# Kernel optimization log

Measured on AMD Instinct MI355X. Metric: run time of the kernel, lower is better.

## Reference

```python
import jax, jax.numpy as jnp
import numpy as np
from jax.scipy.linalg import solve_triangular

T, DZ, DX = 4096, 64, 64


def setup_inputs() -> dict:
    key = jax.random.key(0)
    ks = jax.random.split(key, 8)
    observations = jax.random.normal(ks[0], (T, DX), jnp.float32)
    # stable transition matrix (spectral radius < 1)
    A = 0.9 * jnp.eye(DZ, dtype=jnp.float32) + (0.05 / np.sqrt(DZ)) * jax.random.normal(ks[1], (DZ, DZ), jnp.float32)
    b = 0.01 * jax.random.normal(ks[2], (DZ,), jnp.float32)
    qf = jax.random.normal(ks[3], (DZ, DZ), jnp.float32) / np.sqrt(DZ)
    Q = qf @ qf.T + 0.1 * jnp.eye(DZ, dtype=jnp.float32)  # SPD process noise
    H = jax.random.normal(ks[4], (DX, DZ), jnp.float32) / np.sqrt(DZ)
    c = 0.01 * jax.random.normal(ks[5], (DX,), jnp.float32)
    rf = jax.random.normal(ks[6], (DX, DX), jnp.float32) / np.sqrt(DX)
    R = rf @ rf.T + 0.1 * jnp.eye(DX, dtype=jnp.float32)  # SPD observation noise
    prior_mean = jnp.zeros((DZ,), jnp.float32)
    prior_cov = jnp.eye(DZ, dtype=jnp.float32)
    return dict(observations=observations, A=A, b=b, Q=Q, H=H, c=c, R=R,
                prior_mean=prior_mean, prior_cov=prior_cov)


def _update(m, P, y, H, c, R):
    # Kalman update + Gaussian log-likelihood term (stable Cholesky form of
    # the torch.inverse / MultivariateNormal math).
    yhat = H @ m + c                      # predicted obs mean
    S = H @ P @ H.T + R                   # innovation covariance [dx,dx]
    K = jnp.linalg.solve(S, H @ P).T      # gain = P H^T S^{-1} (S, P symmetric)
    r = y - yhat
    fm = m + K @ r
    fP = P - K @ H @ P
    L = jnp.linalg.cholesky(S)
    z = solve_triangular(L, r, lower=True)
    dx = y.shape[0]
    ll = (-0.5 * dx * jnp.log(2.0 * jnp.pi)
          - jnp.sum(jnp.log(jnp.diag(L)))
          - 0.5 * jnp.sum(z * z))
    return fm, fP, ll


def reference(observations, A, b, Q, H, c, R, prior_mean, prior_cov):
    # ---- filter ----
    fm0, fP0, ll0 = _update(prior_mean, prior_cov, observations[0], H, c, R)

    def fstep(carry, y):
        m, P = carry
        pm = A @ m + b                    # predict
        pP = A @ P @ A.T + Q
        fm, fP, ll = _update(pm, pP, y, H, c, R)
        return (fm, fP), (pm, pP, fm, fP, ll)

    _, (pms, pPs, fms, fPs, lls) = jax.lax.scan(fstep, (fm0, fP0), observations[1:])
    pm = jnp.concatenate([prior_mean[None], pms])   # [T, dz]
    pP = jnp.concatenate([prior_cov[None], pPs])    # [T, dz, dz]
    fm = jnp.concatenate([fm0[None], fms])
    fP = jnp.concatenate([fP0[None], fPs])
    loglikelihood = ll0 + jnp.sum(lls)

    # ---- RTS smoother (backward recursion) ----
    def bstep(carry, xs):
        sm, sP = carry
        fmt, fPt, pmn, pPn = xs
        C = jnp.linalg.solve(pPn, A @ fPt).T          # fP A^T pP^{-1}
        sm_t = fmt + C @ (sm - pmn)
        sP_t = fPt + C @ (sP - pPn) @ C.T
        return (sm_t, sP_t), (sm_t, sP_t)

    _, (sms, sPs) = jax.lax.scan(bstep, (fm[-1], fP[-1]),
                                 (fm[:-1], fP[:-1], pm[1:], pP[1:]), reverse=True)
    smoothed_means = jnp.concatenate([sms, fm[-1][None]])
    smoothed_covs = jnp.concatenate([sPs, fP[-1][None]])
    return smoothed_means, smoothed_covs, loglikelihood
```

## Files before the change

kernel.cpp:

```cpp
#include <hip/hip_runtime.h>
#include <math.h>

#define NN 64
#define LDW 68
#define LCH 32
#define N1CAP 144
#define N0MAX 144
#define EPS_HARD 1e-5f
#define EPS_GATE 5e-2f
#define STALL_WIN 5
#define STALL_IMP 0.75f

struct KP {
  const float *Y, *A, *b, *Q, *H, *c, *R, *pm0, *P0;
  float *out_mean, *out_cov, *out_ll;
  int *meta; float *metaF;
  float *fm;
  float *AT, *HT, *HA, *Hb;
  float *Fss, *Kss, *Sinvss, *Css, *CsTss, *pPss, *sPss, *Fpow, *Cpow32, *Cpow31, *uss;
  float *Pw2, *Pw4, *Pw8, *Pw16, *Pw64, *Pw128;
  float *FpwHi, *CpwHi;
  float *Dmss, *dvnss;
  float *u_chunk, *startstate, *ub_chunk, *endstate;
  float *scanF0, *scanF1, *scanB0, *scanB1;
  float *ld_pref, *u_pref;
  double *llbuf;
  float *E0g;
  float *EA, *EC, *EJ, *EL;
  float *astat, *dstat;
  float *scM0, *scM1, *scG0, *scG1;
  float *fP, *pP, *Kp, *Sinvp, *Fp, *Cp, *CsTp, *Dmp, *dvnp;
  int N0cap, T, NC;
};

union F4 { float4 v; float f[4]; };


__device__ __forceinline__ void g2l(float* W, const float* G) {
  for (int e = threadIdx.x*4; e < 4096; e += 1024) {
    float4 v = *(const float4*)(G + e);
    *(float4*)(W + (e>>6)*LDW + (e&63)) = v;
  }
  __syncthreads();
}
__device__ __forceinline__ void l2g(float* G, const float* W) {
  for (int e = threadIdx.x*4; e < 4096; e += 1024)
    *(float4*)(G + e) = *(const float4*)(W + (e>>6)*LDW + (e&63));
  __syncthreads();
}
__device__ __forceinline__ void l2g2(float* G1, const float* Wa,
                                     float* G2, const float* Wb) {
  for (int e = threadIdx.x*4; e < 4096; e += 1024) {
    int base = (e>>6)*LDW + (e&63);
    *(float4*)(G1 + e) = *(const float4*)(Wa + base);
    *(float4*)(G2 + e) = *(const float4*)(Wb + base);
  }
// ... 699 lines not shown
  const int t = blockIdx.x;
  if (t >= N0) return;
  mm<0,0,0,LDW>(W1, P.H, NN, P.pP + (size_t)t*4096, NN, nullptr, 0);
  mm<0,0,1,LDW>(CH, W1, LDW, P.HT, NN, P.R, NN);
  chol68<true>(CH, part, invd);
  if (tid == 0) { float s=0.f; for (int j=0;j<64;++j) s += part[j]; P.ld_pref[t] = s; }
  set_id(W0);
  tri_s2x2(CH, invd, W1, W0);
  l2g_T(P.Kp + (size_t)t*4096, W1);
  if (tid < 64) {
    float s = P.b[tid];
    for (int k = 0; k < 64; ++k) s -= W1[k*LDW + tid]*P.Hb[k];
    P.u_pref[t*64 + tid] = s;
  }
  __syncthreads();
  l2g(P.Sinvp + (size_t)t*4096, W0);
  mm<1,0,2,LDW>(W0, W1, LDW, P.HA, NN, P.A, NN);
  l2g(P.Fp + (size_t)t*4096, W0);
  mm<0,0,0,LDW>(W1, P.A, NN, P.fP + (size_t)t*4096, NN, nullptr, 0);
  g2l(CH, P.pP + (size_t)(t+1)*4096);
  chol68<false>(CH, part, invd);
  tri_solve2(CH, invd, W1, W1);
  l2g(P.CsTp + (size_t)t*4096, W1);
  l2g_T(P.Cp + (size_t)t*4096, W1);
  mm<1,0,0,LDW>(W0, W1, LDW, P.A, NN, nullptr, 0);
  store_id_sub(P.Dmp + (size_t)t*4096, W0);
  if (tid < 64) {
    float s = 0.f;
    for (int k = 0; k < 64; ++k) s += W1[k*LDW + tid]*P.b[k];
    P.dvnp[t*64 + tid] = -s;
  }
}

__global__ __launch_bounds__(256) void k1y(KP P) {
  __shared__ __align__(16) float W0[LDW*NN], W1[LDW*NN], W2[LDW*NN], W3[LDW*NN], W4[LDW*NN], CH[LDW*NN];
  const int N0 = P.meta[0];
  const float* fPssG = P.fP + (size_t)(N0-1)*4096;
  if (blockIdx.x == 0) {
    mm2<0,0,0,LDW, 0,0,0,LDW>(W1, P.Css,NN, P.Css,NN, nullptr,0,
                              W4, P.Fss,NN, P.Fss,NN, nullptr,0);
    l2g(P.Pw2, W1);
    mm2<0,0,0,LDW, 0,0,0,LDW>(W2, W1,LDW, W1,LDW, nullptr,0,
                              W3, W4,LDW, W4,LDW, nullptr,0);
    l2g(P.Pw4, W2);
    mm2<0,0,0,LDW, 0,0,0,LDW>(W0, W2,LDW, W2,LDW, nullptr,0,
                              W4, W3,LDW, W3,LDW, nullptr,0);
    l2g(P.Pw8, W0);
    mm2<0,0,0,LDW, 0,0,0,LDW>(W1, W0,LDW, W0,LDW, nullptr,0,
                              W3, W4,LDW, W4,LDW, nullptr,0);
    l2g(P.Pw16, W1);
    mm2<0,0,0,LDW, 0,0,0,LDW>(W2, W1,LDW, W1,LDW, nullptr,0,
                              W4, W3,LDW, W3,LDW, nullptr,0);
    l2g2(P.Cpow32, W2, P.Fpow, W4);
    mm2<0,0,0,LDW, 0,0,0,LDW>(W0, W2,LDW, W2,LDW, nullptr,0,
                              W3, W4,LDW, W4,LDW, nullptr,0);
    l2g2(P.Pw64, W0, P.FpwHi, W3);
    mm2<0,0,0,LDW, 0,0,0,LDW>(W1, W0,LDW, W0,LDW, nullptr,0,
                              W4, W3,LDW, W3,LDW, nullptr,0);
    l2g2(P.Pw128, W1, P.FpwHi + 4096, W4);
    mm2<0,0,0,LDW, 0,0,0,LDW>(W2, W1,LDW, W1,LDW, nullptr,0,
                              W3, W4,LDW, W4,LDW, nullptr,0);
    l2g2(P.CpwHi, W2, P.FpwHi + 2*4096, W3);
    mm2<0,0,0,LDW, 0,0,0,LDW>(W0, W2,LDW, W2,LDW, nullptr,0,
                              W4, W3,LDW, W3,LDW, nullptr,0);
    l2g2(P.CpwHi + 4096, W0, P.FpwHi + 3*4096, W4);
    mm2<0,0,0,LDW, 0,0,0,LDW>(W1, W0,LDW, W0,LDW, nullptr,0,
                              W3, W4,LDW, W4,LDW, nullptr,0);
    l2g2(P.CpwHi + 2*4096, W1, P.FpwHi + 4*4096, W3);
    mm2<0,0,0,LDW, 0,0,0,LDW>(W2, W1,LDW, W1,LDW, nullptr,0,
                              W4, W3,LDW, W3,LDW, nullptr,0);
    l2g2(P.CpwHi + 3*4096, W2, P.FpwHi + 5*4096, W4);
    mm<0,0,0,LDW>(W0, P.Pw16, NN, P.Pw8, NN, nullptr, 0);
    mm<0,0,0,LDW>(W1, W0, LDW, P.Pw4, NN, nullptr, 0);
    mm<0,0,0,LDW>(W2, W1, LDW, P.Pw2, NN, nullptr, 0);
    mm<0,0,0,LDW>(W0, W2, LDW, P.Css, NN, nullptr, 0);
    l2g(P.Cpow31, W0);
  } else {
    g2l(W1, P.Css);
    g2l(W2, P.CsTss);
    g2l(W0, P.pPss);
    mm<0,0,0,LDW>(CH, W1, LDW, W0, LDW, nullptr, 0);
    mm<0,0,2,LDW>(W0, CH, LDW, W2, LDW, fPssG, NN);
    float *m1 = W1, *m2 = W2, *t1 = W3, *t2 = W4;
    for (int it = 0; it < 7; ++it) {
      mm2<0,0,0,LDW, 0,0,0,LDW>(CH, m1,LDW, W0,LDW, nullptr,0,
                                t1, m1,LDW, m1,LDW, nullptr,0);
      mm2<0,0,1,LDW, 0,0,0,LDW>(W0, CH,LDW, m2,LDW, W0,LDW,
                                t2, m2,LDW, m2,LDW, nullptr,0);
      float* tmp = m1; m1 = t1; t1 = tmp;
      tmp = m2; m2 = t2; t2 = tmp;
    }
    l2g(P.sPss, W0);
    rsub_store(P.E0g, fPssG, W0);
  }
}

__global__ __launch_bounds__(256) void kTail(KP P) {
  __shared__ __align__(16) float W0[LDW*NN], W1[LDW*NN], W2[LDW*NN];
  const int t = blockIdx.x;
  const int N0 = P.meta[0];
  if (t < N0) return;
  float* dst = P.out_cov + (size_t)t*4096;
  if (t < P.T - N1CAP) {
    for (int e = threadIdx.x*4; e < 4096; e += 1024)
      *(float4*)(dst+e) = *(const float4*)(P.sPss + e);
    return;
  }
  const int k = P.T - 1 - t;
  if (k == 0) {
    const float* src = P.fP + (size_t)(N0-1)*4096;
    for (int e = threadIdx.x*4; e < 4096; e += 1024)
      *(float4*)(dst+e) = *(const float4*)(src+e);
    return;
  }
  const float* pw[8] = {P.Css, P.Pw2, P.Pw4, P.Pw8, P.Pw16, P.Cpow32, P.Pw64, P.Pw128};
  int b = __ffs(k) - 1;
  g2l(W1, pw[b]);
  float* cur = W1; float* oth = W0;
  for (int j = b+1; j < 8; ++j) {
    if ((k >> j) & 1) {
      mm<0,0,0,LDW>(oth, pw[j], NN, cur, LDW, nullptr, 0);
      float* tmp = cur; cur = oth; oth = tmp;
    }
  }
  mm<0,0,0,LDW>(W2, cur, LDW, P.E0g, NN, nullptr, 0);
  mm<0,1,1,LDW>(oth, W2, LDW, cur, LDW, P.sPss, NN);
  l2g(dst, oth);
}

__global__ __launch_bounds__(256) void k1cI(KP P) {
  __shared__ __align__(16) float W1[LDW*NN];
  const int t = blockIdx.x;
  if (t >= P.meta[0]) return;
  const float* Cg = P.Cp + (size_t)t*4096;
  for (int e = threadIdx.x*4; e < 4096; e += 1024)
    *(float4*)(P.scM0 + (size_t)t*4096 + e) = *(const float4*)(Cg + e);
  mm<0,0,0,LDW>(W1, Cg, NN, P.pP + (size_t)(t+1)*4096, NN, nullptr, 0);
  mm<0,0,2,NN>(P.scG0 + (size_t)t*4096, W1, LDW,
               P.CsTp + (size_t)t*4096, NN, P.fP + (size_t)t*4096, NN);
}

__global__ __launch_bounds__(256) void k1cL(KP P, int step, int sidx) {
  __shared__ __align__(16) float W1[LDW*NN];
  const int t = blockIdx.x;
  const int N0 = P.meta[0];
  if (t >= N0) return;
  const float* Msrc = sidx ? P.scM1 : P.scM0;
  const float* Gsrc = sidx ? P.scG1 : P.scG0;
  float* Mdst = sidx ? P.scM0 : P.scM1;
  float* Gdst = sidx ? P.scG0 : P.scG1;
  const int s = t + step;
  if (s >= N0) {
    for (int e = threadIdx.x*4; e < 4096; e += 1024) {
      *(float4*)(Mdst + (size_t)t*4096 + e) = *(const float4*)(Msrc + (size_t)t*4096 + e);
      *(float4*)(Gdst + (size_t)t*4096 + e) = *(const float4*)(Gsrc + (size_t)t*4096 + e);
    }
    return;
  }
  const float* Mt = Msrc + (size_t)t*4096;
  mm2<0,0,0,LDW, 0,0,0,NN>(W1, Mt,NN, Gsrc + (size_t)s*4096,NN, nullptr,0,
                           Mdst + (size_t)t*4096, Mt,NN, Msrc + (size_t)s*4096,NN, nullptr,0);
  mm<0,1,1,NN>(Gdst + (size_t)t*4096, W1, LDW, Mt, NN, Gsrc + (size_t)t*4096, NN);
}

__global__ __launch_bounds__(256) void k1cF(KP P) {
  __shared__ __align__(16) float W1[LDW*NN];
  const int t = blockIdx.x;
  if (t >= P.meta[0]) return;
  const float* Mt = P.scM0 + (size_t)t*4096;
  mm<0,0,0,LDW>(W1, Mt, NN, P.sPss, NN, nullptr, 0);
  mm<0,1,1,NN>(P.out_cov + (size_t)t*4096, W1, LDW, Mt, NN,
               P.scG0 + (size_t)t*4096, NN);
}

__global__ __launch_bounds__(256) void k2a(KP P) {
  __shared__ float xv[64], ty[64], red[256];
  const int c = blockIdx.x;
  const int N0 = P.meta[0];
  const int PB = (N0 + LCH - 1)/LCH;
  if (c < PB) return;
  const int tid = threadIdx.x;
  if (tid < 64) xv[tid] = 0.f;
  __syncthreads();
  for (int s = 0; s < LCH; ++s) {
    int t = c*LCH + s;
    if (tid < 64) ty[tid] = P.Y[(size_t)t*64+tid] - P.c[tid];
    __syncthreads();
    matvec2(xv, P.Fss, xv, P.Kss, ty, P.uss, red);
  }
  if (tid < 64) P.scanF0[(size_t)(c+1)*64 + tid] = xv[tid];
}

__global__ __launch_bounds__(256) void k2b(KP P) {
  __shared__ float xv[64], ty[64], hp[64], red[256];
  const int tid = threadIdx.x;
  const int N0 = P.meta[0];
  const int PB = (N0 + LCH - 1)/LCH;
  const int PE = PB*LCH;
  if (tid < 64) xv[tid] = P.pm0[tid];
  __syncthreads();
  matvec256(hp, P.H, xv, nullptr, red);
  if (tid < 64) ty[tid] = P.Y[tid] - hp[tid] - P.c[tid];
  __syncthreads();
  matvec256(xv, P.Kp, ty, xv, red);
  if (tid < 64) P.fm[tid] = xv[tid];
  __syncthreads();
  for (int t = 1; t < PE; ++t) {
    const float* Kt = (t < N0) ? P.Kp + (size_t)t*4096 : P.Kss;
    const float* Ft = (t < N0) ? P.Fp + (size_t)t*4096 : P.Fss;
    const float* ut = (t < N0) ? P.u_pref + t*64 : P.uss;
    if (tid < 64) ty[tid] = P.Y[(size_t)t*64+tid] - P.c[tid];
    __syncthreads();
    matvec2(xv, Ft, xv, Kt, ty, ut, red);
    if (tid < 64) P.fm[(size_t)t*64+tid] = xv[tid];
    __syncthreads();
  }
  if (tid < 64) P.scanF0[(size_t)PB*64 + tid] = xv[tid];
}

__global__ __launch_bounds__(64) void k2s(KP P, int j) {
  const int c = blockIdx.x;
  const int N0 = P.meta[0];
  const int PB = (N0 + LCH - 1)/LCH;
  if (c < PB) return;
  const int sidx = j & 1;
  const float* src = sidx ? P.scanF1 : P.scanF0;
  float* dst = sidx ? P.scanF0 : P.scanF1;
  const int off = 1 << j;
  const int r = threadIdx.x;
  float base = src[(size_t)c*64 + r];
  if (c - off >= PB) {
    __shared__ float xv[64];
    xv[r] = src[(size_t)(c-off)*64 + r];
    __syncthreads();
    const float* M = (j == 0) ? P.Fpow : P.FpwHi + (size_t)(j-1)*4096;
    const float* Mr = M + r*64;
    float s = base;
    for (int k = 0; k < 64; k += 4)
      s += Mr[k]*xv[k] + Mr[k+1]*xv[k+1] + Mr[k+2]*xv[k+2] + Mr[k+3]*xv[k+3];
    dst[(size_t)c*64 + r] = s;
  } else {
    dst[(size_t)c*64 + r] = base;
  }
}

__global__ __launch_bounds__(256) void k2c(KP P) {
  __shared__ float xv[64], ty[64], red[256];
  const int c = blockIdx.x;
  const int N0 = P.meta[0];
  const int PB = (N0 + LCH - 1)/LCH;
  if (c < PB) return;
  const int tid = threadIdx.x;
  if (tid < 64) xv[tid] = P.scanF1[(size_t)c*64 + tid];
  __syncthreads();
  for (int s = 0; s < LCH; ++s) {
    int t = c*LCH + s;
    if (tid < 64) ty[tid] = P.Y[(size_t)t*64+tid] - P.c[tid];
    __syncthreads();
    matvec2(xv, P.Fss, xv, P.Kss, ty, P.uss, red);
    if (tid < 64) P.fm[(size_t)t*64+tid] = xv[tid];
    __syncthreads();
  }
}

__global__ __launch_bounds__(64) void k5(KP P) {
  __shared__ float pmv[64], rv[64];
  const int t = blockIdx.x;
  const int N0 = P.meta[0];
  const int r = threadIdx.x;
  float pm;
  if (t == 0) {
    pm = P.pm0[r];
  } else {
    pmv[r] = P.fm[(size_t)(t-1)*64 + r];
    __syncthreads();
    float s = P.b[r];
    const float* Ar = P.A + r*64;
    for (int k = 0; k < 64; k += 4)
      s += Ar[k]*pmv[k] + Ar[k+1]*pmv[k+1] + Ar[k+2]*pmv[k+2] + Ar[k+3]*pmv[k+3];
    pm = s;
    __syncthreads();
  }
  pmv[r] = pm; __syncthreads();
  float rr = P.Y[(size_t)t*64 + r] - P.c[r];
  const float* Hr = P.H + r*64;
  for (int k = 0; k < 64; ++k) rr -= Hr[k]*pmv[k];
  rv[r] = rr; __syncthreads();
  const float* Sv = ((t < N0) ? P.Sinvp + (size_t)t*4096 : P.Sinvss) + r*64;
  float wv = 0.f;
  for (int k = 0; k < 64; ++k) wv += Sv[k]*rv[k];
  float qq = rr*wv;
  #pragma unroll
  for (int off = 32; off > 0; off >>= 1) qq += __shfl_xor(qq, off, 64);
  if (r == 0) {
    float ldt = (t < N0) ? P.ld_pref[t] : P.metaF[0];
    P.llbuf[t] = -58.8120661250990555 - (double)ldt - 0.5*(double)qq;
  }
}

__global__ __launch_bounds__(256) void k3a(KP P) {
  __shared__ float sv[64], fmv[64], red[256];
  const int c = blockIdx.x;
  const int N0 = P.meta[0];
  const int PB = (N0 + LCH - 1)/LCH;
  if (c < PB) return;
  const int tid = threadIdx.x;
  if (tid < 64) sv[tid] = 0.f;
  __syncthreads();
  int hi = (c == P.NC-1) ? P.T-2 : c*LCH + LCH - 1;
  for (int t = hi; t >= c*LCH; --t) {
    if (tid < 64) fmv[tid] = P.fm[(size_t)t*64+tid];
    __syncthreads();
    matvec2(sv, P.Css, sv, P.Dmss, fmv, P.dvnss, red);
  }
  if (c == P.NC-1) {
    if (tid < 64) fmv[tid] = P.fm[(size_t)(P.T-1)*64 + tid];
    __syncthreads();
    matvec256(sv, P.Cpow31, fmv, sv, red);
  }
  if (tid < 64) P.scanB0[(size_t)c*64 + tid] = sv[tid];
}

__global__ __launch_bounds__(64) void k3s(KP P, int j) {
  const int c = blockIdx.x;
  const int N0 = P.meta[0];
  const int PB = (N0 + LCH - 1)/LCH;
  if (c < PB) return;
  const int sidx = j & 1;
  const float* src = sidx ? P.scanB1 : P.scanB0;
  float* dst = sidx ? P.scanB0 : P.scanB1;
  const int off = 1 << j;
  const int r = threadIdx.x;
  float base = src[(size_t)c*64 + r];
  if (c + off <= P.NC - 1) {
    __shared__ float xv[64];
    xv[r] = src[(size_t)(c+off)*64 + r];
    __syncthreads();
    const float* M;
    if (j == 0) M = P.Cpow32;
    else if (j == 1) M = P.Pw64;
    else if (j == 2) M = P.Pw128;
    else M = P.CpwHi + (size_t)(j-3)*4096;
    const float* Mr = M + r*64;
    float s = base;
    for (int k = 0; k < 64; k += 4)
      s += Mr[k]*xv[k] + Mr[k+1]*xv[k+1] + Mr[k+2]*xv[k+2] + Mr[k+3]*xv[k+3];
    dst[(size_t)c*64 + r] = s;
  } else {
    dst[(size_t)c*64 + r] = base;
  }
}

__global__ __launch_bounds__(256) void k3b(KP P) {
  __shared__ float sv[64], fmv[64], red[256];
  const int tid = threadIdx.x;
  const int N0 = P.meta[0];
  const int PB = (N0 + LCH - 1)/LCH;
  const int PE = PB*LCH;
  if (tid < 64) {
    P.out_mean[(size_t)(P.T-1)*64+tid] = P.fm[(size_t)(P.T-1)*64+tid];
    sv[tid] = P.scanB1[(size_t)PB*64 + tid];
  }
  __syncthreads();
  for (int t = PE-1; t >= 0; --t) {
    const float* Ct  = (t < N0) ? P.Cp  + (size_t)t*4096 : P.Css;
    const float* Dmt = (t < N0) ? P.Dmp + (size_t)t*4096 : P.Dmss;
    const float* dvt = (t < N0) ? P.dvnp + t*64 : P.dvnss;
    if (tid < 64) fmv[tid] = P.fm[(size_t)t*64+tid];
    __syncthreads();
    matvec2(sv, Ct, sv, Dmt, fmv, dvt, red);
    if (tid < 64) P.out_mean[(size_t)t*64+tid] = sv[tid];
    __syncthreads();
  }
}

__global__ __launch_bounds__(256) void k3c(KP P) {
  __shared__ float sv[64], fmv[64], red[256];
  const int c = blockIdx.x;
  const int N0 = P.meta[0];
  const int PB = (N0 + LCH - 1)/LCH;
  if (c < PB) return;
  const int tid = threadIdx.x;
  if (tid < 64) {
    sv[tid] = (c == P.NC-1) ? P.fm[(size_t)(P.T-1)*64+tid]
                            : P.scanB1[(size_t)(c+1)*64 + tid];
  }
  __syncthreads();
  int hi = (c == P.NC-1) ? P.T-2 : c*LCH + LCH - 1;
  for (int t = hi; t >= c*LCH; --t) {
    if (tid < 64) fmv[tid] = P.fm[(size_t)t*64+tid];
    __syncthreads();
    matvec2(sv, P.Css, sv, P.Dmss, fmv, P.dvnss, red);
    if (tid < 64) P.out_mean[(size_t)t*64+tid] = sv[tid];
    __syncthreads();
  }
}

__global__ __launch_bounds__(256) void k6(KP P) {
  __shared__ double rd[256];
  double s = 0.0;
  for (int t = threadIdx.x; t < P.T; t += 256) s += P.llbuf[t];
  rd[threadIdx.x] = s; __syncthreads();
  #pragma unroll
  for (int off = 128; off > 0; off >>= 1) {
    if ((int)threadIdx.x < off) rd[threadIdx.x] += rd[threadIdx.x + off];
    __syncthreads();
  }
  if (threadIdx.x == 0) P.out_ll[0] = (float)rd[0];
}


extern "C" void kernel_launch(void* const* d_in, const int* in_sizes, int n_in,
                              void* d_out, int out_size, void* d_ws, size_t ws_size,
                              hipStream_t stream) {
  (void)n_in; (void)out_size;
  KP P;
  P.Y   = (const float*)d_in[0];
  P.A   = (const float*)d_in[1];
  P.b   = (const float*)d_in[2];
  P.Q   = (const float*)d_in[3];
  P.H   = (const float*)d_in[4];
  P.c   = (const float*)d_in[5];
  P.R   = (const float*)d_in[6];
  P.pm0 = (const float*)d_in[7];
  P.P0  = (const float*)d_in[8];
  const int T = in_sizes[0] / 64;
  const int NC = T / LCH;
  P.T = T; P.NC = NC;

  float* out = (float*)d_out;
  P.out_mean = out;
  P.out_cov  = out + (size_t)T*64;
  P.out_ll   = out + (size_t)T*64 + (size_t)T*4096;

  float* w = (float*)d_ws;
  size_t off = 0;
  auto alloc = [&](size_t n) { float* p = w + off; off += n; return p; };
  P.meta   = (int*)alloc(8);
  P.metaF  = alloc(8);
  P.llbuf  = (double*)alloc((size_t)2*T);
  P.fm     = alloc((size_t)T*64);
  P.AT = alloc(4096); P.HT = alloc(4096); P.HA = alloc(4096); P.Hb = alloc(64);
  P.Fss = alloc(4096); P.Kss = alloc(4096); P.Sinvss = alloc(4096);
  P.Css = alloc(4096); P.CsTss = alloc(4096); P.pPss = alloc(4096); P.sPss = alloc(4096);
  P.Fpow = alloc(4096); P.Cpow32 = alloc(4096); P.Cpow31 = alloc(4096); P.uss = alloc(64);
  P.Pw2 = alloc(4096); P.Pw4 = alloc(4096); P.Pw8 = alloc(4096); P.Pw16 = alloc(4096);
  P.Pw64 = alloc(4096); P.Pw128 = alloc(4096);
  P.FpwHi = alloc((size_t)6*4096); P.CpwHi = alloc((size_t)4*4096);
  P.Dmss = alloc(4096); P.dvnss = alloc(64);
  P.u_chunk = alloc((size_t)NC*64); P.startstate = alloc((size_t)NC*64);
  P.ub_chunk = alloc((size_t)NC*64); P.endstate = alloc((size_t)NC*64);
  P.scanF0 = alloc((size_t)(NC+1)*64); P.scanF1 = alloc((size_t)(NC+1)*64);
  P.scanB0 = alloc((size_t)NC*64); P.scanB1 = alloc((size_t)NC*64);
  P.E0g = alloc(4096);
  P.EA = alloc((size_t)8*4096); P.EC = alloc((size_t)8*4096);
  P.EJ = alloc((size_t)8*4096); P.EL = alloc((size_t)8*4096);
  P.astat = alloc(256); P.dstat = alloc(256);
  size_t fixed = off;
  size_t per_t = 12*4096 + 128 + 1;
  size_t total_f = ws_size / 4;
  long long avail = (long long)total_f - (long long)fixed - 4096 - 64;
  int cap = (avail > 0) ? (int)(avail / (long long)per_t) : 8;
  if (cap > N0MAX) cap = N0MAX;
  if (cap < 8) cap = 8;
  P.N0cap = cap;
  P.ld_pref = alloc(cap);
  P.u_pref  = alloc((size_t)cap*64);
  P.dvnp    = alloc((size_t)cap*64);
  P.fP    = alloc((size_t)cap*4096);
  P.pP    = alloc((size_t)(cap+1)*4096);
  P.Kp    = alloc((size_t)cap*4096);
  P.Sinvp = alloc((size_t)cap*4096);
  P.Fp    = alloc((size_t)cap*4096);
  P.Cp    = alloc((size_t)cap*4096);
  P.CsTp  = alloc((size_t)cap*4096);
  P.Dmp   = alloc((size_t)cap*4096);
  P.scM0  = alloc((size_t)cap*4096);
  P.scM1  = alloc((size_t)cap*4096);
  P.scG0  = alloc((size_t)cap*4096);
  P.scG1  = alloc((size_t)cap*4096);

  k0<<<1, 256, 0, stream>>>(P);
  kA<<<1, 256, 0, stream>>>(P);
  kB<<<cap, 256, 0, stream>>>(P);
  kC<<<cap, 256, 0, stream>>>(P);
  kN<<<1, 256, 0, stream>>>(P);
  k1x<<<cap+1, 256, 0, stream>>>(P);
  k1y<<<2, 256, 0, stream>>>(P);
  k1cI<<<cap, 256, 0, stream>>>(P);
  {
    int sidx = 0;
    for (int d = 0; d < 8; ++d) { k1cL<<<cap, 256, 0, stream>>>(P, 1 << d, sidx); sidx ^= 1; }
  }
  k1cF<<<cap, 256, 0, stream>>>(P);
  kTail<<<T, 256, 0, stream>>>(P);
  k2a<<<NC, 256, 0, stream>>>(P);
  k2b<<<1, 256, 0, stream>>>(P);
  for (int j = 0; j < 7; ++j) k2s<<<NC, 64, 0, stream>>>(P, j);
  k2c<<<NC, 256, 0, stream>>>(P);
  k5<<<T, 64, 0, stream>>>(P);
  k3a<<<NC, 256, 0, stream>>>(P);
  for (int j = 0; j < 7; ++j) k3s<<<NC, 64, 0, stream>>>(P, j);
  k3b<<<1, 256, 0, stream>>>(P);
  k3c<<<NC, 256, 0, stream>>>(P);
  k6<<<1, 256, 0, stream>>>(P);
}
```

Measured before the change: 1.794 ms.

## Merge independent smoother and filter stages into combined multi-role kernels

Independent phases (power precomputation, steady-state covariance, chunked forward filter, covariance scan init, the prefix-scan levels, tail covariances, log-likelihood terms, backward smoother and final reduction) are packed into shared launches. Different block-index ranges take different roles, so independent work runs concurrently and roughly 30 launches shrink to about 18. Some previously parallel work now shares a launch with long serial single-block loops (the forward filter recursion now sits in the first combined kernel). Every block also reserves the largest shared-memory footprint, which may lower occupancy, and the larger grids add idle early-exit blocks.

Result: faster. 1.511 ms (median of 2 runs) (-15.8%).

```diff
diff --git a/kernel.cpp b/kernel.cpp
--- a/kernel.cpp
+++ b/kernel.cpp
@@ -21,7 +21,6 @@
   float *Pw2, *Pw4, *Pw8, *Pw16, *Pw64, *Pw128;
   float *FpwHi, *CpwHi;
   float *Dmss, *dvnss;
-  float *u_chunk, *startstate, *ub_chunk, *endstate;
   float *scanF0, *scanF1, *scanB0, *scanB1;
   float *ld_pref, *u_pref;
   double *llbuf;
@@ -787,293 +786,313 @@
   }
 }
 
-__global__ __launch_bounds__(256) void k1y(KP P) {
+__global__ __launch_bounds__(256) void mega0(KP P) {
   __shared__ __align__(16) float W0[LDW*NN], W1[LDW*NN], W2[LDW*NN], W3[LDW*NN], W4[LDW*NN], CH[LDW*NN];
-  const int N0 = P.meta[0];
-  const float* fPssG = P.fP + (size_t)(N0-1)*4096;
-  if (blockIdx.x == 0) {
-    mm2<0,0,0,LDW, 0,0,0,LDW>(W1, P.Css,NN, P.Css,NN, nullptr,0,
-                              W4, P.Fss,NN, P.Fss,NN, nullptr,0);
-    l2g(P.Pw2, W1);
-    mm2<0,0,0,LDW, 0,0,0,LDW>(W2, W1,LDW, W1,LDW, nullptr,0,
-                              W3, W4,LDW, W4,LDW, nullptr,0);
-    l2g(P.Pw4, W2);
-    mm2<0,0,0,LDW, 0,0,0,LDW>(W0, W2,LDW, W2,LDW, nullptr,0,
-                              W4, W3,LDW, W3,LDW, nullptr,0);
-    l2g(P.Pw8, W0);
-    mm2<0,0,0,LDW, 0,0,0,LDW>(W1, W0,LDW, W0,LDW, nullptr,0,
-                              W3, W4,LDW, W4,LDW, nullptr,0);
-    l2g(P.Pw16, W1);
-    mm2<0,0,0,LDW, 0,0,0,LDW>(W2, W1,LDW, W1,LDW, nullptr,0,
-                              W4, W3,LDW, W3,LDW, nullptr,0);
-    l2g2(P.Cpow32, W2, P.Fpow, W4);
-    mm2<0,0,0,LDW, 0,0,0,LDW>(W0, W2,LDW, W2,LDW, nullptr,0,
-                              W3, W4,LDW, W4,LDW, nullptr,0);
-    l2g2(P.Pw64, W0, P.FpwHi, W3);
-    mm2<0,0,0,LDW, 0,0,0,LDW>(W1, W0,LDW, W0,LDW, nullptr,0,
-                              W4, W3,LDW, W3,LDW, nullptr,0);
-    l2g2(P.Pw128, W1, P.FpwHi + 4096, W4);
-    mm2<0,0,0,LDW, 0,0,0,LDW>(W2, W1,LDW, W1,LDW, nullptr,0,
-                              W3, W4,LDW, W4,LDW, nullptr,0);
-    l2g2(P.CpwHi, W2, P.FpwHi + 2*4096, W3);
-    mm2<0,0,0,LDW, 0,0,0,LDW>(W0, W2,LDW, W2,LDW, nullptr,0,
-                              W4, W3,LDW, W3,LDW, nullptr,0);
-    l2g2(P.CpwHi + 4096, W0, P.FpwHi + 3*4096, W4);
-    mm2<0,0,0,LDW, 0,0,0,LDW>(W1, W0,LDW, W0,LDW, nullptr,0,
-                              W3, W4,LDW, W4,LDW, nullptr,0);
-    l2g2(P.CpwHi + 2*4096, W1, P.FpwHi + 4*4096, W3);
-    mm2<0,0,0,LDW, 0,0,0,LDW>(W2, W1,LDW, W1,LDW, nullptr,0,
-                              W4, W3,LDW, W3,LDW, nullptr,0);
-    l2g2(P.CpwHi + 3*4096, W2, P.FpwHi + 5*4096, W4);
-    mm<0,0,0,LDW>(W0, P.Pw16, NN, P.Pw8, NN, nullptr, 0);
-    mm<0,0,0,LDW>(W1, W0, LDW, P.Pw4, NN, nullptr, 0);
-    mm<0,0,0,LDW>(W2, W1, LDW, P.Pw2, NN, nullptr, 0);
-    mm<0,0,0,LDW>(W0, W2, LDW, P.Css, NN, nullptr, 0);
-    l2g(P.Cpow31, W0);
-  } else {
-    g2l(W1, P.Css);
-    g2l(W2, P.CsTss);
-    g2l(W0, P.pPss);
-    mm<0,0,0,LDW>(CH, W1, LDW, W0, LDW, nullptr, 0);
-    mm<0,0,2,LDW>(W0, CH, LDW, W2, LDW, fPssG, NN);
-    float *m1 = W1, *m2 = W2, *t1 = W3, *t2 = W4;
-    for (int it = 0; it < 7; ++it) {
-      mm2<0,0,0,LDW, 0,0,0,LDW>(CH, m1,LDW, W0,LDW, nullptr,0,
-                                t1, m1,LDW, m1,LDW, nullptr,0);
-      mm2<0,0,1,LDW, 0,0,0,LDW>(W0, CH,LDW, m2,LDW, W0,LDW,
-                                t2, m2,LDW, m2,LDW, nullptr,0);
-      float* tmp = m1; m1 = t1; t1 = tmp;
-      tmp = m2; m2 = t2; t2 = tmp;
-    }
-    l2g(P.sPss, W0);
-    rsub_store(P.E0g, fPssG, W0);
-  }
-}
-
-__global__ __launch_bounds__(256) void kTail(KP P) {
-  __shared__ __align__(16) float W0[LDW*NN], W1[LDW*NN], W2[LDW*NN];
-  const int t = blockIdx.x;
-  const int N0 = P.meta[0];
-  if (t < N0) return;
-  float* dst = P.out_cov + (size_t)t*4096;
-  if (t < P.T - N1CAP) {
-    for (int e = threadIdx.x*4; e < 4096; e += 1024)
-      *(float4*)(dst+e) = *(const float4*)(P.sPss + e);
-    return;
-  }
-  const int k = P.T - 1 - t;
-  if (k == 0) {
-    const float* src = P.fP + (size_t)(N0-1)*4096;
-    for (int e = threadIdx.x*4; e < 4096; e += 1024)
-      *(float4*)(dst+e) = *(const float4*)(src+e);
-    return;
-  }
-  const float* pw[8] = {P.Css, P.Pw2, P.Pw4, P.Pw8, P.Pw16, P.Cpow32, P.Pw64, P.Pw128};
-  int b = __ffs(k) - 1;
-  g2l(W1, pw[b]);
-  float* cur = W1; float* oth = W0;
-  for (int j = b+1; j < 8; ++j) {
-    if ((k >> j) & 1) {
-      mm<0,0,0,LDW>(oth, pw[j], NN, cur, LDW, nullptr, 0);
-      float* tmp = cur; cur = oth; oth = tmp;
-    }
-  }
-  mm<0,0,0,LDW>(W2, cur, LDW, P.E0g, NN, nullptr, 0);
-  mm<0,1,1,LDW>(oth, W2, LDW, cur, LDW, P.sPss, NN);
-  l2g(dst, oth);
-}
-
-__global__ __launch_bounds__(256) void k1cI(KP P) {
-  __shared__ __align__(16) float W1[LDW*NN];
-  const int t = blockIdx.x;
-  if (t >= P.meta[0]) return;
-  const float* Cg = P.Cp + (size_t)t*4096;
-  for (int e = threadIdx.x*4; e < 4096; e += 1024)
-    *(float4*)(P.scM0 + (size_t)t*4096 + e) = *(const float4*)(Cg + e);
-  mm<0,0,0,LDW>(W1, Cg, NN, P.pP + (size_t)(t+1)*4096, NN, nullptr, 0);
-  mm<0,0,2,NN>(P.scG0 + (size_t)t*4096, W1, LDW,
-               P.CsTp + (size_t)t*4096, NN, P.fP + (size_t)t*4096, NN);
-}
-
-__global__ __launch_bounds__(256) void k1cL(KP P, int step, int sidx) {
-  __shared__ __align__(16) float W1[LDW*NN];
-  const int t = blockIdx.x;
-  const int N0 = P.meta[0];
-  if (t >= N0) return;
-  const float* Msrc = sidx ? P.scM1 : P.scM0;
-  const float* Gsrc = sidx ? P.scG1 : P.scG0;
-  float* Mdst = sidx ? P.scM0 : P.scM1;
-  float* Gdst = sidx ? P.scG0 : P.scG1;
-  const int s = t + step;
-  if (s >= N0) {
-    for (int e = threadIdx.x*4; e < 4096; e += 1024) {
-      *(float4*)(Mdst + (size_t)t*4096 + e) = *(const float4*)(Msrc + (size_t)t*4096 + e);
-      *(float4*)(Gdst + (size_t)t*4096 + e) = *(const float4*)(Gsrc + (size_t)t*4096 + e);
-    }
-    return;
-  }
-  const float* Mt = Msrc + (size_t)t*4096;
-  mm2<0,0,0,LDW, 0,0,0,NN>(W1, Mt,NN, Gsrc + (size_t)s*4096,NN, nullptr,0,
-                           Mdst + (size_t)t*4096, Mt,NN, Msrc + (size_t)s*4096,NN, nullptr,0);
-  mm<0,1,1,NN>(Gdst + (size_t)t*4096, W1, LDW, Mt, NN, Gsrc + (size_t)t*4096, NN);
-}
-
-__global__ __launch_bounds__(256) void k1cF(KP P) {
-  __shared__ __align__(16) float W1[LDW*NN];
-  const int t = blockIdx.x;
-  if (t >= P.meta[0]) return;
-  const float* Mt = P.scM0 + (size_t)t*4096;
-  mm<0,0,0,LDW>(W1, Mt, NN, P.sPss, NN, nullptr, 0);
-  mm<0,1,1,NN>(P.out_cov + (size_t)t*4096, W1, LDW, Mt, NN,
-               P.scG0 + (size_t)t*4096, NN);
-}
-
-__global__ __launch_bounds__(256) void k2a(KP P) {
-  __shared__ float xv[64], ty[64], red[256];
-  const int c = blockIdx.x;
+  __shared__ float xv[64], ty[64], hp[64], red[256];
+  const int tid = threadIdx.x;
+  const int bid = blockIdx.x;
   const int N0 = P.meta[0];
   const int PB = (N0 + LCH - 1)/LCH;
-  if (c < PB) return;
+  if (bid == 0) {
+    const int PE = PB*LCH;
+    if (tid < 64) xv[tid] = P.pm0[tid];
+    __syncthreads();
+    matvec256(hp, P.H, xv, nullptr, red);
+    if (tid < 64) ty[tid] = P.Y[tid] - hp[tid] - P.c[tid];
+    __syncthreads();
+    matvec256(xv, P.Kp, ty, xv, red);
+    if (tid < 64) P.fm[tid] = xv[tid];
+    __syncthreads();
+    for (int t = 1; t < PE; ++t) {
+      const float* Kt = (t < N0) ? P.Kp + (size_t)t*4096 : P.Kss;
+      const float* Ft = (t < N0) ? P.Fp + (size_t)t*4096 : P.Fss;
+      const float* ut = (t < N0) ? P.u_pref + t*64 : P.uss;
+      if (tid < 64) ty[tid] = P.Y[(size_t)t*64+tid] - P.c[tid];
+      __syncthreads();
+      matvec2(xv, Ft, xv, Kt, ty, ut, red);
+      if (tid < 64) P.fm[(size_t)t*64+tid] = xv[tid];
+      __syncthreads();
+    }
+    if (tid < 64) P.scanF0[(size_t)PB*64 + tid] = xv[tid];
+  } else if (bid <= 2) {
+    const float* fPssG = P.fP + (size_t)(N0-1)*4096;
+    if (bid == 1) {
+      mm2<0,0,0,LDW, 0,0,0,LDW>(W1, P.Css,NN, P.Css,NN, nullptr,0,
+                                W4, P.Fss,NN, P.Fss,NN, nullptr,0);
+      l2g(P.Pw2, W1);
+      mm2<0,0,0,LDW, 0,0,0,LDW>(W2, W1,LDW, W1,LDW, nullptr,0,
+                                W3, W4,LDW, W4,LDW, nullptr,0);
+      l2g(P.Pw4, W2);
+      mm2<0,0,0,LDW, 0,0,0,LDW>(W0, W2,LDW, W2,LDW, nullptr,0,
+                                W4, W3,LDW, W3,LDW, nullptr,0);
+      l2g(P.Pw8, W0);
+      mm2<0,0,0,LDW, 0,0,0,LDW>(W1, W0,LDW, W0,LDW, nullptr,0,
+                                W3, W4,LDW, W4,LDW, nullptr,0);
+      l2g(P.Pw16, W1);
+      mm2<0,0,0,LDW, 0,0,0,LDW>(W2, W1,LDW, W1,LDW, nullptr,0,
+                                W4, W3,LDW, W3,LDW, nullptr,0);
+      l2g2(P.Cpow32, W2, P.Fpow, W4);
+      mm2<0,0,0,LDW, 0,0,0,LDW>(W0, W2,LDW, W2,LDW, nullptr,0,
+                                W3, W4,LDW, W4,LDW, nullptr,0);
+      l2g2(P.Pw64, W0, P.FpwHi, W3);
+      mm2<0,0,0,LDW, 0,0,0,LDW>(W1, W0,LDW, W0,LDW, nullptr,0,
+                                W4, W3,LDW, W3,LDW, nullptr,0);
+      l2g2(P.Pw128, W1, P.FpwHi + 4096, W4);
+      mm2<0,0,0,LDW, 0,0,0,LDW>(W2, W1,LDW, W1,LDW, nullptr,0,
+                                W3, W4,LDW, W4,LDW, nullptr,0);
+      l2g2(P.CpwHi, W2, P.FpwHi + 2*4096, W3);
+      mm2<0,0,0,LDW, 0,0,0,LDW>(W0, W2,LDW, W2,LDW, nullptr,0,
+                                W4, W3,LDW, W3,LDW, nullptr,0);
+      l2g2(P.CpwHi + 4096, W0, P.FpwHi + 3*4096, W4);
+      mm2<0,0,0,LDW, 0,0,0,LDW>(W1, W0,LDW, W0,LDW, nullptr,0,
+                                W3, W4,LDW, W4,LDW, nullptr,0);
+      l2g2(P.CpwHi + 2*4096, W1, P.FpwHi + 4*4096, W3);
+      mm2<0,0,0,LDW, 0,0,0,LDW>(W2, W1,LDW, W1,LDW, nullptr,0,
+                                W4, W3,LDW, W3,LDW, nullptr,0);
+      l2g2(P.CpwHi + 3*4096, W2, P.FpwHi + 5*4096, W4);
+      mm<0,0,0,LDW>(W0, P.Pw16, NN, P.Pw8, NN, nullptr, 0);
+      mm<0,0,0,LDW>(W1, W0, LDW, P.Pw4, NN, nullptr, 0);
+      mm<0,0,0,LDW>(W2, W1, LDW, P.Pw2, NN, nullptr, 0);
+      mm<0,0,0,LDW>(W0, W2, LDW, P.Css, NN, nullptr, 0);
+      l2g(P.Cpow31, W0);
+    } else {
+      g2l(W1, P.Css);
+      g2l(W2, P.CsTss);
+      g2l(W0, P.pPss);
+      mm<0,0,0,LDW>(CH, W1, LDW, W0, LDW, nullptr, 0);
+      mm<0,0,2,LDW>(W0, CH, LDW, W2, LDW, fPssG, NN);
+      float *m1 = W1, *m2 = W2, *t1 = W3, *t2 = W4;
+      for (int it = 0; it < 7; ++it) {
+        mm2<0,0,0,LDW, 0,0,0,LDW>(CH, m1,LDW, W0,LDW, nullptr,0,
+                                  t1, m1,LDW, m1,LDW, nullptr,0);
+        mm2<0,0,1,LDW, 0,0,0,LDW>(W0, CH,LDW, m2,LDW, W0,LDW,
+                                  t2, m2,LDW, m2,LDW, nullptr,0);
+        float* tmp = m1; m1 = t1; t1 = tmp;
+        tmp = m2; m2 = t2; t2 = tmp;
+      }
+      l2g(P.sPss, W0);
+      rsub_store(P.E0g, fPssG, W0);
+    }
+  } else if (bid < 3 + P.NC) {
+    const int c = bid - 3;
+    if (c < PB) return;
+    if (tid < 64) xv[tid] = 0.f;
+    __syncthreads();
+    for (int s = 0; s < LCH; ++s) {
+      int t = c*LCH + s;
+      if (tid < 64) ty[tid] = P.Y[(size_t)t*64+tid] - P.c[tid];
+      __syncthreads();
+      matvec2(xv, P.Fss, xv, P.Kss, ty, P.uss, red);
+    }
+    if (tid < 64) P.scanF0[(size_t)(c+1)*64 + tid] = xv[tid];
+  } else {
+    const int t = bid - 3 - P.NC;
+    if (t >= N0) return;
+    const float* Cg = P.Cp + (size_t)t*4096;
+    for (int e = tid*4; e < 4096; e += 1024)
+      *(float4*)(P.scM0 + (size_t)t*4096 + e) = *(const float4*)(Cg + e);
+    mm<0,0,0,LDW>(W1, Cg, NN, P.pP + (size_t)(t+1)*4096, NN, nullptr, 0);
+    mm<0,0,2,NN>(P.scG0 + (size_t)t*4096, W1, LDW,
+                 P.CsTp + (size_t)t*4096, NN, P.fP + (size_t)t*4096, NN);
+  }
+}
+
+__global__ __launch_bounds__(256) void megaL(KP P, int d) {
+  __shared__ __align__(16) float W1[LDW*NN];
+  __shared__ float xv[64];
   const int tid = threadIdx.x;
-  if (tid < 64) xv[tid] = 0.f;
-  __syncthreads();
-  for (int s = 0; s < LCH; ++s) {
-    int t = c*LCH + s;
-    if (tid < 64) ty[tid] = P.Y[(size_t)t*64+tid] - P.c[tid];
-    __syncthreads();
-    matvec2(xv, P.Fss, xv, P.Kss, ty, P.uss, red);
-  }
-  if (tid < 64) P.scanF0[(size_t)(c+1)*64 + tid] = xv[tid];
-}
-
-__global__ __launch_bounds__(256) void k2b(KP P) {
-  __shared__ float xv[64], ty[64], hp[64], red[256];
+  const int bid = blockIdx.x;
+  const int cap = P.N0cap;
+  const int N0 = P.meta[0];
+  if (bid < cap) {
+    const int t = bid;
+    if (t >= N0) return;
+    const int step = 1 << d, sidx = d & 1;
+    const float* Msrc = sidx ? P.scM1 : P.scM0;
+    const float* Gsrc = sidx ? P.scG1 : P.scG0;
+    float* Mdst = sidx ? P.scM0 : P.scM1;
+    float* Gdst = sidx ? P.scG0 : P.scG1;
+    const int s = t + step;
+    if (s >= N0) {
+      for (int e = tid*4; e < 4096; e += 1024) {
+        *(float4*)(Mdst + (size_t)t*4096 + e) = *(const float4*)(Msrc + (size_t)t*4096 + e);
+        *(float4*)(Gdst + (size_t)t*4096 + e) = *(const float4*)(Gsrc + (size_t)t*4096 + e);
+      }
+      return;
+    }
+    const float* Mt = Msrc + (size_t)t*4096;
+    mm2<0,0,0,LDW, 0,0,0,NN>(W1, Mt,NN, Gsrc + (size_t)s*4096,NN, nullptr,0,
+                             Mdst + (size_t)t*4096, Mt,NN, Msrc + (size_t)s*4096,NN, nullptr,0);
+    mm<0,1,1,NN>(Gdst + (size_t)t*4096, W1, LDW, Mt, NN, Gsrc + (size_t)t*4096, NN);
+  } else {
+    const int c = bid - cap;
+    const int PB = (N0 + LCH - 1)/LCH;
+    if (c < PB) return;
+    const int sidx = d & 1;
+    const float* src = sidx ? P.scanF1 : P.scanF0;
+    float* dst = sidx ? P.scanF0 : P.scanF1;
+    const int off = 1 << d;
+    const int r = tid;
+    if (c - off >= PB) {
+      if (r < 64) xv[r] = src[(size_t)(c-off)*64 + r];
+      __syncthreads();
+      if (r < 64) {
+        const float* M = (d == 0) ? P.Fpow : P.FpwHi + (size_t)(d-1)*4096;
+        const float* Mr = M + r*64;
+        float s = src[(size_t)c*64 + r];
+        for (int k = 0; k < 64; k += 4)
+          s += Mr[k]*xv[k] + Mr[k+1]*xv[k+1] + Mr[k+2]*xv[k+2] + Mr[k+3]*xv[k+3];
+        dst[(size_t)c*64 + r] = s;
+      }
+    } else {
+      if (r < 64) dst[(size_t)c*64 + r] = src[(size_t)c*64 + r];
+    }
+  }
+}
+
+__global__ __launch_bounds__(256) void megaL7(KP P) {
+  __shared__ __align__(16) float W1[LDW*NN];
+  __shared__ float xv[64], ty[64], red[256];
   const int tid = threadIdx.x;
+  const int bid = blockIdx.x;
   const int N0 = P.meta[0];
   const int PB = (N0 + LCH - 1)/LCH;
-  const int PE = PB*LCH;
-  if (tid < 64) xv[tid] = P.pm0[tid];
-  __syncthreads();
-  matvec256(hp, P.H, xv, nullptr, red);
-  if (tid < 64) ty[tid] = P.Y[tid] - hp[tid] - P.c[tid];
-  __syncthreads();
-  matvec256(xv, P.Kp, ty, xv, red);
-  if (tid < 64) P.fm[tid] = xv[tid];
-  __syncthreads();
-  for (int t = 1; t < PE; ++t) {
-    const float* Kt = (t < N0) ? P.Kp + (size_t)t*4096 : P.Kss;
-    const float* Ft = (t < N0) ? P.Fp + (size_t)t*4096 : P.Fss;
-    const float* ut = (t < N0) ? P.u_pref + t*64 : P.uss;
-    if (tid < 64) ty[tid] = P.Y[(size_t)t*64+tid] - P.c[tid];
-    __syncthreads();
-    matvec2(xv, Ft, xv, Kt, ty, ut, red);
-    if (tid < 64) P.fm[(size_t)t*64+tid] = xv[tid];
-    __syncthreads();
-  }
-  if (tid < 64) P.scanF0[(size_t)PB*64 + tid] = xv[tid];
-}
-
-__global__ __launch_bounds__(64) void k2s(KP P, int j) {
-  const int c = blockIdx.x;
+  if (bid < P.NC) {
+    const int c = bid;
+    if (c < PB) return;
+    if (tid < 64) xv[tid] = P.scanF1[(size_t)c*64 + tid];
+    __syncthreads();
+    for (int s = 0; s < LCH; ++s) {
+      int t = c*LCH + s;
+      if (tid < 64) ty[tid] = P.Y[(size_t)t*64+tid] - P.c[tid];
+      __syncthreads();
+      matvec2(xv, P.Fss, xv, P.Kss, ty, P.uss, red);
+      if (tid < 64) P.fm[(size_t)t*64+tid] = xv[tid];
+      __syncthreads();
+    }
+  } else {
+    const int t = bid - P.NC;
+    if (t >= N0) return;
+    const int step = 128, sidx = 1;
+    const float* Msrc = sidx ? P.scM1 : P.scM0;
+    const float* Gsrc = sidx ? P.scG1 : P.scG0;
+    float* Mdst = sidx ? P.scM0 : P.scM1;
+    float* Gdst = sidx ? P.scG0 : P.scG1;
+    const int s = t + step;
+    if (s >= N0) {
+      for (int e = tid*4; e < 4096; e += 1024) {
+        *(float4*)(Mdst + (size_t)t*4096 + e) = *(const float4*)(Msrc + (size_t)t*4096 + e);
+        *(float4*)(Gdst + (size_t)t*4096 + e) = *(const float4*)(Gsrc + (size_t)t*4096 + e);
+      }
+      return;
+    }
+    const float* Mt = Msrc + (size_t)t*4096;
+    mm2<0,0,0,LDW, 0,0,0,NN>(W1, Mt,NN, Gsrc + (size_t)s*4096,NN, nullptr,0,
+                             Mdst + (size_t)t*4096, Mt,NN, Msrc + (size_t)s*4096,NN, nullptr,0);
+    mm<0,1,1,NN>(Gdst + (size_t)t*4096, W1, LDW, Mt, NN, Gsrc + (size_t)t*4096, NN);
+  }
+}
+
+__global__ __launch_bounds__(256) void mega2(KP P) {
+  __shared__ __align__(16) float W0[LDW*NN], W1[LDW*NN], W2[LDW*NN];
+  __shared__ float sv[64], fmv[64], red[256];
+  const int tid = threadIdx.x;
+  const int bid = blockIdx.x;
+  const int NC = P.NC, cap = P.N0cap, T = P.T;
   const int N0 = P.meta[0];
   const int PB = (N0 + LCH - 1)/LCH;
-  if (c < PB) return;
-  const int sidx = j & 1;
-  const float* src = sidx ? P.scanF1 : P.scanF0;
-  float* dst = sidx ? P.scanF0 : P.scanF1;
-  const int off = 1 << j;
-  const int r = threadIdx.x;
-  float base = src[(size_t)c*64 + r];
-  if (c - off >= PB) {
-    __shared__ float xv[64];
-    xv[r] = src[(size_t)(c-off)*64 + r];
-    __syncthreads();
-    const float* M = (j == 0) ? P.Fpow : P.FpwHi + (size_t)(j-1)*4096;
-    const float* Mr = M + r*64;
-    float s = base;
-    for (int k = 0; k < 64; k += 4)
-      s += Mr[k]*xv[k] + Mr[k+1]*xv[k+1] + Mr[k+2]*xv[k+2] + Mr[k+3]*xv[k+3];
-    dst[(size_t)c*64 + r] = s;
+  if (bid < NC) {
+    const int c = bid;
+    if (c < PB) return;
+    if (tid < 64) sv[tid] = 0.f;
+    __syncthreads();
+    int hi = (c == NC-1) ? T-2 : c*LCH + LCH - 1;
+    for (int t = hi; t >= c*LCH; --t) {
+      if (tid < 64) fmv[tid] = P.fm[(size_t)t*64+tid];
+      __syncthreads();
+      matvec2(sv, P.Css, sv, P.Dmss, fmv, P.dvnss, red);
+    }
+    if (c == NC-1) {
+      if (tid < 64) fmv[tid] = P.fm[(size_t)(T-1)*64 + tid];
+      __syncthreads();
+      matvec256(sv, P.Cpow31, fmv, sv, red);
+    }
+    if (tid < 64) P.scanB0[(size_t)c*64 + tid] = sv[tid];
+  } else if (bid < NC + T) {
+    const int t = bid - NC;
+    if (t < N0) return;
+    float* dst = P.out_cov + (size_t)t*4096;
+    if (t < T - N1CAP) {
+      for (int e = tid*4; e < 4096; e += 1024)
+        *(float4*)(dst+e) = *(const float4*)(P.sPss + e);
+      return;
+    }
+    const int k = T - 1 - t;
+    if (k == 0) {
+      const float* src = P.fP + (size_t)(N0-1)*4096;
+      for (int e = tid*4; e < 4096; e += 1024)
+        *(float4*)(dst+e) = *(const float4*)(src+e);
+      return;
+    }
+    const float* pw[8] = {P.Css, P.Pw2, P.Pw4, P.Pw8, P.Pw16, P.Cpow32, P.Pw64, P.Pw128};
+    int b = __ffs(k) - 1;
+    g2l(W1, pw[b]);
+    float* cur = W1; float* oth = W0;
+    for (int j = b+1; j < 8; ++j) {
+      if ((k >> j) & 1) {
+        mm<0,0,0,LDW>(oth, pw[j], NN, cur, LDW, nullptr, 0);
+        float* tmp = cur; cur = oth; oth = tmp;
+      }
+    }
+    mm<0,0,0,LDW>(W2, cur, LDW, P.E0g, NN, nullptr, 0);
+    mm<0,1,1,LDW>(oth, W2, LDW, cur, LDW, P.sPss, NN);
+    l2g(dst, oth);
+  } else if (bid < NC + T + cap) {
+    const int t = bid - NC - T;
+    if (t >= N0) return;
+    const float* Mt = P.scM0 + (size_t)t*4096;
+    mm<0,0,0,LDW>(W1, Mt, NN, P.sPss, NN, nullptr, 0);
+    mm<0,1,1,NN>(P.out_cov + (size_t)t*4096, W1, LDW, Mt, NN,
+                 P.scG0 + (size_t)t*4096, NN);
   } else {
-    dst[(size_t)c*64 + r] = base;
-  }
-}
-
-__global__ __launch_bounds__(256) void k2c(KP P) {
-  __shared__ float xv[64], ty[64], red[256];
-  const int c = blockIdx.x;
-  const int N0 = P.meta[0];
-  const int PB = (N0 + LCH - 1)/LCH;
-  if (c < PB) return;
-  const int tid = threadIdx.x;
-  if (tid < 64) xv[tid] = P.scanF1[(size_t)c*64 + tid];
-  __syncthreads();
-  for (int s = 0; s < LCH; ++s) {
-    int t = c*LCH + s;
-    if (tid < 64) ty[tid] = P.Y[(size_t)t*64+tid] - P.c[tid];
-    __syncthreads();
-    matvec2(xv, P.Fss, xv, P.Kss, ty, P.uss, red);
-    if (tid < 64) P.fm[(size_t)t*64+tid] = xv[tid];
-    __syncthreads();
-  }
-}
-
-__global__ __launch_bounds__(64) void k5(KP P) {
-  __shared__ float pmv[64], rv[64];
-  const int t = blockIdx.x;
-  const int N0 = P.meta[0];
-  const int r = threadIdx.x;
-  float pm;
-  if (t == 0) {
-    pm = P.pm0[r];
-  } else {
-    pmv[r] = P.fm[(size_t)(t-1)*64 + r];
-    __syncthreads();
-    float s = P.b[r];
-    const float* Ar = P.A + r*64;
-    for (int k = 0; k < 64; k += 4)
-      s += Ar[k]*pmv[k] + Ar[k+1]*pmv[k+1] + Ar[k+2]*pmv[k+2] + Ar[k+3]*pmv[k+3];
-    pm = s;
-    __syncthreads();
-  }
-  pmv[r] = pm; __syncthreads();
-  float rr = P.Y[(size_t)t*64 + r] - P.c[r];
-  const float* Hr = P.H + r*64;
-  for (int k = 0; k < 64; ++k) rr -= Hr[k]*pmv[k];
-  rv[r] = rr; __syncthreads();
-  const float* Sv = ((t < N0) ? P.Sinvp + (size_t)t*4096 : P.Sinvss) + r*64;
-  float wv = 0.f;
-  for (int k = 0; k < 64; ++k) wv += Sv[k]*rv[k];
-  float qq = rr*wv;
-  #pragma unroll
-  for (int off = 32; off > 0; off >>= 1) qq += __shfl_xor(qq, off, 64);
-  if (r == 0) {
-    float ldt = (t < N0) ? P.ld_pref[t] : P.metaF[0];
-    P.llbuf[t] = -58.8120661250990555 - (double)ldt - 0.5*(double)qq;
-  }
-}
-
-__global__ __launch_bounds__(256) void k3a(KP P) {
-  __shared__ float sv[64], fmv[64], red[256];
-  const int c = blockIdx.x;
-  const int N0 = P.meta[0];
-  const int PB = (N0 + LCH - 1)/LCH;
-  if (c < PB) return;
-  const int tid = threadIdx.x;
-  if (tid < 64) sv[tid] = 0.f;
-  __syncthreads();
-  int hi = (c == P.NC-1) ? P.T-2 : c*LCH + LCH - 1;
-  for (int t = hi; t >= c*LCH; --t) {
-    if (tid < 64) fmv[tid] = P.fm[(size_t)t*64+tid];
-    __syncthreads();
-    matvec2(sv, P.Css, sv, P.Dmss, fmv, P.dvnss, red);
-  }
-  if (c == P.NC-1) {
-    if (tid < 64) fmv[tid] = P.fm[(size_t)(P.T-1)*64 + tid];
-    __syncthreads();
-    matvec256(sv, P.Cpow31, fmv, sv, red);
-  }
-  if (tid < 64) P.scanB0[(size_t)c*64 + tid] = sv[tid];
+    const int t = bid - NC - T - cap;
+    const int r = tid;
+    if (t == 0) {
+      if (r < 64) fmv[r] = P.pm0[r];
+      __syncthreads();
+    } else {
+      if (r < 64) sv[r] = P.fm[(size_t)(t-1)*64 + r];
+      __syncthreads();
+      if (r < 64) {
+        float s = P.b[r];
+        const float* Ar = P.A + r*64;
+        for (int k = 0; k < 64; k += 4)
+          s += Ar[k]*sv[k] + Ar[k+1]*sv[k+1] + Ar[k+2]*sv[k+2] + Ar[k+3]*sv[k+3];
+        fmv[r] = s;
+      }
+      __syncthreads();
+    }
+    float qq = 0.f;
+    if (r < 64) {
+      float rr = P.Y[(size_t)t*64 + r] - P.c[r];
+      const float* Hr = P.H + r*64;
+      for (int k = 0; k < 64; ++k) rr -= Hr[k]*fmv[k];
+      sv[r] = rr;
+    }
+    __syncthreads();
+    if (r < 64) {
+      const float* Sv = ((t < N0) ? P.Sinvp + (size_t)t*4096 : P.Sinvss) + r*64;
+      float wv = 0.f;
+      for (int k = 0; k < 64; ++k) wv += Sv[k]*sv[k];
+      qq = sv[r]*wv;
+      #pragma unroll
+      for (int off = 32; off > 0; off >>= 1) qq += __shfl_xor(qq, off, 64);
+      if (r == 0) {
+        float ldt = (t < N0) ? P.ld_pref[t] : P.metaF[0];
+        P.llbuf[t] = -58.8120661250990555 - (double)ldt - 0.5*(double)qq;
+      }
+    }
+  }
 }
 
 __global__ __launch_bounds__(64) void k3s(KP P, int j) {
@@ -1106,62 +1125,57 @@
   }
 }
 
-__global__ __launch_bounds__(256) void k3b(KP P) {
+__global__ __launch_bounds__(256) void mega3(KP P) {
   __shared__ float sv[64], fmv[64], red[256];
+  __shared__ double rd[256];
   const int tid = threadIdx.x;
+  const int bid = blockIdx.x;
   const int N0 = P.meta[0];
   const int PB = (N0 + LCH - 1)/LCH;
-  const int PE = PB*LCH;
-  if (tid < 64) {
-    P.out_mean[(size_t)(P.T-1)*64+tid] = P.fm[(size_t)(P.T-1)*64+tid];
-    sv[tid] = P.scanB1[(size_t)PB*64 + tid];
-  }
-  __syncthreads();
-  for (int t = PE-1; t >= 0; --t) {
-    const float* Ct  = (t < N0) ? P.Cp  + (size_t)t*4096 : P.Css;
-    const float* Dmt = (t < N0) ? P.Dmp + (size_t)t*4096 : P.Dmss;
-    const float* dvt = (t < N0) ? P.dvnp + t*64 : P.dvnss;
-    if (tid < 64) fmv[tid] = P.fm[(size_t)t*64+tid];
-    __syncthreads();
-    matvec2(sv, Ct, sv, Dmt, fmv, dvt, red);
-    if (tid < 64) P.out_mean[(size_t)t*64+tid] = sv[tid];
-    __syncthreads();
-  }
-}
-
-__global__ __launch_bounds__(256) void k3c(KP P) {
-  __shared__ float sv[64], fmv[64], red[256];
-  const int c = blockIdx.x;
-  const int N0 = P.meta[0];
-  const int PB = (N0 + LCH - 1)/LCH;
-  if (c < PB) return;
-  const int tid = threadIdx.x;
-  if (tid < 64) {
-    sv[tid] = (c == P.NC-1) ? P.fm[(size_t)(P.T-1)*64+tid]
-                            : P.scanB1[(size_t)(c+1)*64 + tid];
-  }
-  __syncthreads();
-  int hi = (c == P.NC-1) ? P.T-2 : c*LCH + LCH - 1;
-  for (int t = hi; t >= c*LCH; --t) {
-    if (tid < 64) fmv[tid] = P.fm[(size_t)t*64+tid];
-    __syncthreads();
-    matvec2(sv, P.Css, sv, P.Dmss, fmv, P.dvnss, red);
-    if (tid < 64) P.out_mean[(size_t)t*64+tid] = sv[tid];
-    __syncthreads();
-  }
-}
-
-__global__ __launch_bounds__(256) void k6(KP P) {
-  __shared__ double rd[256];
-  double s = 0.0;
-  for (int t = threadIdx.x; t < P.T; t += 256) s += P.llbuf[t];
-  rd[threadIdx.x] = s; __syncthreads();
-  #pragma unroll
-  for (int off = 128; off > 0; off >>= 1) {
-    if ((int)threadIdx.x < off) rd[threadIdx.x] += rd[threadIdx.x + off];
-    __syncthreads();
-  }
-  if (threadIdx.x == 0) P.out_ll[0] = (float)rd[0];
+  if (bid == 0) {
+    const int PE = PB*LCH;
+    if (tid < 64) {
+      P.out_mean[(size_t)(P.T-1)*64+tid] = P.fm[(size_t)(P.T-1)*64+tid];
+      sv[tid] = P.scanB1[(size_t)PB*64 + tid];
+    }
+    __syncthreads();
+    for (int t = PE-1; t >= 0; --t) {
+      const float* Ct  = (t < N0) ? P.Cp  + (size_t)t*4096 : P.Css;
+      const float* Dmt = (t < N0) ? P.Dmp + (size_t)t*4096 : P.Dmss;
+      const float* dvt = (t < N0) ? P.dvnp + t*64 : P.dvnss;
+      if (tid < 64) fmv[tid] = P.fm[(size_t)t*64+tid];
+      __syncthreads();
+      matvec2(sv, Ct, sv, Dmt, fmv, dvt, red);
+      if (tid < 64) P.out_mean[(size_t)t*64+tid] = sv[tid];
+      __syncthreads();
+    }
+  } else if (bid <= P.NC) {
+    const int c = bid - 1;
+    if (c < PB) return;
+    if (tid < 64) {
+      sv[tid] = (c == P.NC-1) ? P.fm[(size_t)(P.T-1)*64+tid]
+                              : P.scanB1[(size_t)(c+1)*64 + tid];
+    }
+    __syncthreads();
+    int hi = (c == P.NC-1) ? P.T-2 : c*LCH + LCH - 1;
+    for (int t = hi; t >= c*LCH; --t) {
+      if (tid < 64) fmv[tid] = P.fm[(size_t)t*64+tid];
+      __syncthreads();
+      matvec2(sv, P.Css, sv, P.Dmss, fmv, P.dvnss, red);
+      if (tid < 64) P.out_mean[(size_t)t*64+tid] = sv[tid];
+      __syncthreads();
+    }
+  } else {
+    double s = 0.0;
+    for (int t = tid; t < P.T; t += 256) s += P.llbuf[t];
+    rd[tid] = s; __syncthreads();
+    #pragma unroll
+    for (int off = 128; off > 0; off >>= 1) {
+      if (tid < off) rd[tid] += rd[tid + off];
+      __syncthreads();
+    }
+    if (tid == 0) P.out_ll[0] = (float)rd[0];
+  }
 }
 
 
@@ -1203,8 +1217,6 @@
   P.Pw64 = alloc(4096); P.Pw128 = alloc(4096);
   P.FpwHi = alloc((size_t)6*4096); P.CpwHi = alloc((size_t)4*4096);
   P.Dmss = alloc(4096); P.dvnss = alloc(64);
-  P.u_chunk = alloc((size_t)NC*64); P.startstate = alloc((size_t)NC*64);
-  P.ub_chunk = alloc((size_t)NC*64); P.endstate = alloc((size_t)NC*64);
   P.scanF0 = alloc((size_t)(NC+1)*64); P.scanF1 = alloc((size_t)(NC+1)*64);
   P.scanB0 = alloc((size_t)NC*64); P.scanB1 = alloc((size_t)NC*64);
   P.E0g = alloc(4096);
@@ -1241,22 +1253,12 @@
   kC<<<cap, 256, 0, stream>>>(P);
   kN<<<1, 256, 0, stream>>>(P);
   k1x<<<cap+1, 256, 0, stream>>>(P);
-  k1y<<<2, 256, 0, stream>>>(P);
-  k1cI<<<cap, 256, 0, stream>>>(P);
-  {
-    int sidx = 0;
-    for (int d = 0; d < 8; ++d) { k1cL<<<cap, 256, 0, stream>>>(P, 1 << d, sidx); sidx ^= 1; }
-  }
-  k1cF<<<cap, 256, 0, stream>>>(P);
-  kTail<<<T, 256, 0, stream>>>(P);
-  k2a<<<NC, 256, 0, stream>>>(P);
-  k2b<<<1, 256, 0, stream>>>(P);
-  for (int j = 0; j < 7; ++j) k2s<<<NC, 64, 0, stream>>>(P, j);
-  k2c<<<NC, 256, 0, stream>>>(P);
-  k5<<<T, 64, 0, stream>>>(P);
-  k3a<<<NC, 256, 0, stream>>>(P);
-  for (int j = 0; j < 7; ++j) k3s<<<NC, 64, 0, stream>>>(P, j);
-  k3b<<<1, 256, 0, stream>>>(P);
-  k3c<<<NC, 256, 0, stream>>>(P);
-  k6<<<1, 256, 0, stream>>>(P);
-}
+  mega0<<<3 + NC + cap, 256, 0, stream>>>(P);
+  for (int d = 0; d < 7; ++d)
+    megaL<<<cap + NC, 256, 0, stream>>>(P, d);
+  megaL7<<<NC + cap, 256, 0, stream>>>(P);
+  mega2<<<NC + T + cap + T, 256, 0, stream>>>(P);
+  for (int j = 0; j < 7; ++j)
+    k3s<<<NC, 64, 0, stream>>>(P, j);
+  mega3<<<NC + 2, 256, 0, stream>>>(P);
+}
```
